# Performance work log

Measured on AMD Instinct MI355X. Metric: run time of the kernel, lower is better.

## Reference

```python
import jax, jax.numpy as jnp
import numpy as np

K = 20
BN_INV = float(1.0 / np.sqrt(1.0 + 1e-5))  # BatchNorm eval with running_mean=0, running_var=1


def _leaky(h):
    return jnp.where(h >= 0, h, 0.2 * h)


def _knn_idx(x, k):
    # x: [B, C, N]; pairwise_distance = -(||xi||^2 + ||xj||^2 - 2 xi.xj); topk = nearest
    inner = jnp.einsum('bcn,bcm->bnm', x, x)
    xx = jnp.sum(x * x, axis=1)  # [B, N]
    pd = 2.0 * inner - xx[:, :, None] - xx[:, None, :]
    return jax.lax.top_k(pd, k)[1]  # [B, N, k]


def _edge_conv(x, w, g, b, k):
    # x: [B, C, N]; w: [Cout, 2C]
    idx = _knn_idx(x, k)
    xt = jnp.transpose(x, (0, 2, 1))  # [B, N, C]
    nb = jax.vmap(lambda f, i: f[i])(xt, idx)  # [B, N, k, C] gathered neighbors
    ctr = xt[:, :, None, :]
    feat = jnp.concatenate([nb - ctr, jnp.broadcast_to(ctr, nb.shape)], axis=-1)  # [B,N,k,2C]
    h = jnp.einsum('bnkc,oc->bnko', feat, w)
    h = _leaky(g * h * BN_INV + b)
    h = jnp.max(h, axis=2)  # max over k neighbors -> [B, N, Cout]
    return jnp.transpose(h, (0, 2, 1))  # [B, Cout, N]


def setup_inputs() -> dict:
    key = jax.random.key(0)
    ks = jax.random.split(key, 32)
    s = 0.05

    def w(i, shape):
        return jax.random.normal(ks[i], shape, dtype=jnp.float32) * s

    def gb(i, c):
        return (1.0 + 0.1 * jax.random.normal(ks[i], (c,), dtype=jnp.float32),
                0.1 * jax.random.normal(jax.random.fold_in(ks[i], 1), (c,), dtype=jnp.float32))

    g1, b1 = gb(1, 64); g2, b2 = gb(2, 64); g3, b3 = gb(3, 128); g4, b4 = gb(4, 256)
    gc, bc = gb(5, 1024); gf1, bf1 = gb(6, 512); gf2, bf2 = gb(7, 256)
    return {
        'x': jax.random.normal(ks[0], (8, 3, 2048), dtype=jnp.float32),
        'w1': w(8, (64, 6)),   'g1': g1, 'b1': b1,
        'w2': w(9, (64, 128)), 'g2': g2, 'b2': b2,
        'w3': w(10, (128, 128)), 'g3': g3, 'b3': b3,
        'w4': w(11, (256, 256)), 'g4': g4, 'b4': b4,
        'wc': w(12, (1024, 512)), 'gc': gc, 'bc': bc,
        'wf1': w(13, (512, 2048)), 'gf1': gf1, 'bf1': bf1,
        'wf2': w(14, (256, 512)), 'bwf2': w(15, (256,)), 'gf2': gf2, 'bf2': bf2,
        'wf3': w(16, (40, 256)), 'bwf3': w(17, (40,)),
    }


def reference(x, w1, g1, b1, w2, g2, b2, w3, g3, b3, w4, g4, b4,
              wc, gc, bc, wf1, gf1, bf1, wf2, bwf2, gf2, bf2, wf3, bwf3):
    x1 = _edge_conv(x, w1, g1, b1, K)   # [B, 64, N]
    x2 = _edge_conv(x1, w2, g2, b2, K)  # [B, 64, N]
    x3 = _edge_conv(x2, w3, g3, b3, K)  # [B, 128, N]
    x4 = _edge_conv(x3, w4, g4, b4, K)  # [B, 256, N]
    h = jnp.concatenate([x1, x2, x3, x4], axis=1)  # [B, 512, N]
    h = jnp.einsum('bcn,oc->bon', h, wc)
    h = _leaky(gc[:, None] * h * BN_INV + bc[:, None])  # [B, 1024, N]
    x5 = jnp.max(h, axis=2)
    x6 = jnp.mean(h, axis=2)
    h = jnp.concatenate([x5, x6], axis=1)  # [B, 2048]
    h = _leaky(gf1 * (h @ wf1.T) * BN_INV + bf1)   # fc1 (no bias) + BN + LeakyReLU
    h = _leaky(gf2 * (h @ wf2.T + bwf2) * BN_INV + bf2)  # fc2 + BN + LeakyReLU (dropout=eval identity)
    return h @ wf3.T + bwf3  # [B, numClass]
```

## Files before the change

kernel.cpp:

```cpp
#include <hip/hip_runtime.h>
#include <hip/hip_bf16.h>
#include <float.h>

#define BB 8
#define NN 2048
#define KK 20

static constexpr float BN_INV_F = 0.9999950000374997f;

typedef __attribute__((ext_vector_type(4))) float f32x4;
typedef __attribute__((ext_vector_type(8))) short s16x8;

__device__ __forceinline__ unsigned short f2bf(float f) {
    __hip_bfloat16 h = __float2bfloat16(f);
    return __builtin_bit_cast(unsigned short, h);
}
__device__ __forceinline__ float bf2f(unsigned short u) {
    unsigned int v = ((unsigned int)u) << 16;
    return __builtin_bit_cast(float, v);
}
__device__ __forceinline__ unsigned mono(float f) {
    unsigned b = __builtin_bit_cast(unsigned, f);
    return b ^ (unsigned)(((int)b >> 31) | 0x80000000);
}

__global__ void split_kernel(const float* __restrict__ w, unsigned short* __restrict__ hi,
                             unsigned short* __restrict__ lo, int n) {
    int t = blockIdx.x * blockDim.x + threadIdx.x;
    if (t >= n) return;
    float v = w[t];
    unsigned short h = f2bf(v);
    hi[t] = h;
    lo[t] = f2bf(v - bf2f(h));
}

__global__ void sqnorm_kernel(const float* __restrict__ x, float* __restrict__ xx, int C) {
    int t = blockIdx.x * blockDim.x + threadIdx.x;
    if (t >= BB * NN) return;
    int b = t / NN, n = t % NN;
    const float* xb = x + (size_t)b * C * NN + n;
    float s = 0.f;
    for (int c = 0; c < C; ++c) {
        float v = xb[(size_t)c * NN];
        s += v * v;
    }
    xx[t] = s;
}

__global__ __launch_bounds__(256, 4) void pd_kernel(const float* __restrict__ x,
                                                    const float* __restrict__ xx,
                                                    float* __restrict__ pd,
                                                    int C, int baseB) {
    __shared__ float ctrT[128][8];
    __shared__ float xns[8];

    int blk = blockIdx.x;
    int chalf = blk & 1;
    int rt = (blk >> 1) & 255;
    int b2 = blk >> 9;
    int b = baseB + b2;
    int rbase = rt * 8;
    int tid = threadIdx.x;
    const float* xb = x + (size_t)b * C * NN;

    for (int i = tid; i < C * 8; i += 256) {
        int c = i >> 3, r = i & 7;
        ctrT[c][r] = xb[(size_t)c * NN + rbase + r];
    }
    if (tid < 8) xns[tid] = xx[b * NN + rbase + tid];
    __syncthreads();

    int m0 = chalf * 1024 + tid * 4;
    float acc[8][4];
    #pragma unroll
    for (int r = 0; r < 8; ++r)
        #pragma unroll
        for (int j = 0; j < 4; ++j) acc[r][j] = 0.f;

    f32x4 xv = *(const f32x4*)(xb + m0);
    for (int c = 0; c + 1 < C; ++c) {
        f32x4 nxt = *(const f32x4*)(xb + (size_t)(c + 1) * NN + m0);
        f32x4 c0 = *(const f32x4*)&ctrT[c][0];
        f32x4 c1 = *(const f32x4*)&ctrT[c][4];
        #pragma unroll
        for (int j = 0; j < 4; ++j) {
            acc[0][j] += c0.x * xv[j]; acc[1][j] += c0.y * xv[j];
            acc[2][j] += c0.z * xv[j]; acc[3][j] += c0.w * xv[j];
            acc[4][j] += c1.x * xv[j]; acc[5][j] += c1.y * xv[j];
            acc[6][j] += c1.z * xv[j]; acc[7][j] += c1.w * xv[j];
        }
        xv = nxt;
    }
    {
        f32x4 c0 = *(const f32x4*)&ctrT[C - 1][0];
        f32x4 c1 = *(const f32x4*)&ctrT[C - 1][4];
        #pragma unroll
        for (int j = 0; j < 4; ++j) {
            acc[0][j] += c0.x * xv[j]; acc[1][j] += c0.y * xv[j];
            acc[2][j] += c0.z * xv[j]; acc[3][j] += c0.w * xv[j];
            acc[4][j] += c1.x * xv[j]; acc[5][j] += c1.y * xv[j];
            acc[6][j] += c1.z * xv[j]; acc[7][j] += c1.w * xv[j];
        }
    }
    f32x4 xm = *(const f32x4*)(xx + (size_t)b * NN + m0);
    #pragma unroll
    for (int r = 0; r < 8; ++r) {
        f32x4 out;
        #pragma unroll
        for (int j = 0; j < 4; ++j)
            out[j] = 2.f * acc[r][j] - xns[r] - xm[j];
        *(f32x4*)&pd[((size_t)(b2 * NN + rbase + r)) * NN + m0] = out;
    }
}

__global__ __launch_bounds__(256, 4) void topk_kernel(const float* __restrict__ pd,
                                                      int* __restrict__ idxout, int baseB) {
    __shared__ unsigned long long cand[4][128];
    int w = threadIdx.x >> 6, lane = threadIdx.x & 63;
    int rowc = blockIdx.x * 4 + w;
    const float* prow = pd + (size_t)rowc * NN;

    float fv[32];
    #pragma unroll
    for (int j4 = 0; j4 < 8; ++j4) {
        f32x4 v = *(const f32x4*)(prow + j4 * 256 + lane * 4);
        #pragma unroll
        for (int e = 0; e < 4; ++e) fv[j4 * 4 + e] = v[e];
    }

    float lm = fv[0];
    #pragma unroll
    for (int i = 1; i < 32; ++i) lm = fmaxf(lm, fv[i]);

    float v = lm;
    #pragma unroll
    for (int k = 2; k <= 64; k <<= 1)
        #pragma unroll
        for (int j = k >> 1; j > 0; j >>= 1) {
            float o = __shfl_xor(v, j, 64);
            bool up = ((lane & k) == 0);
            bool keepMax = up ? ((lane & j) == 0) : ((lane & j) != 0);
            float mx = fmaxf(v, o), mn = fminf(v, o);
            v = keepMax ? mx : mn;
        }
    float Tf = __shfl(v, KK - 1, 64);

    cand[w][lane] = 0ull;
    cand[w][64 + lane] = 0ull;
    __builtin_amdgcn_wave_barrier();
    int base = 0;
    #pragma unroll
    for (int i = 0; i < 32; ++i) {
        int col = (i >> 2) * 256 + lane * 4 + (i & 3);
        bool c = fv[i] >= Tf;
        unsigned long long mask = __ballot(c);
        if (c) {
            int pos = base + (int)__popcll(mask & ((1ull << lane) - 1ull));
            if (pos < 128)
                cand[w][pos] = ((unsigned long long)mono(fv[i]) << 32) | (unsigned)~col;
        }
        base += (int)__popcll(mask);
    }
    __builtin_amdgcn_wave_barrier();

    unsigned long long ka = cand[w][lane];
    auto cmpx = [&](unsigned long long& key, int j, bool up) {
        unsigned long long o = __shfl_xor(key, j, 64);
        bool keepMax = up ? ((lane & j) == 0) : ((lane & j) != 0);
        bool gt = key > o;
        unsigned long long mx = gt ? key : o, mn = gt ? o : key;
        key = keepMax ? mx : mn;
    };
    if (base <= 64) {
        #pragma unroll
        for (int k = 2; k <= 64; k <<= 1)
            #pragma unroll
            for (int j = k >> 1; j > 0; j >>= 1)
                cmpx(ka, j, (lane & k) == 0);
    } else {
        unsigned long long kb = cand[w][64 + lane];
        #pragma unroll
        for (int k = 2; k <= 128; k <<= 1) {
            #pragma unroll
            for (int j = k >> 1; j > 0; j >>= 1) {
                if (j == 64) {
                    unsigned long long mx = ka > kb ? ka : kb;
                    unsigned long long mn = ka > kb ? kb : ka;
                    ka = mx; kb = mn;
                } else {
                    bool upA, upB;
                    if (k == 128)     { upA = true; upB = true; }
                    else if (k == 64) { upA = true; upB = false; }
                    else              { upA = ((lane & k) == 0); upB = upA; }
                    cmpx(ka, j, upA);
                    cmpx(kb, j, upB);
                }
            }
        }
    }

    if (lane < KK) {
        int col = (int)~(unsigned)(ka & 0xFFFFFFFFull);
        int b = baseB + (rowc >> 11);
        int n = rowc & 2047;
        idxout[((size_t)(b * NN + n)) * KK + lane] = col;
    }
}

__global__ __launch_bounds__(256) void pq_gemm_kernel(const float* __restrict__ x,
                                                      const float* __restrict__ w,
                                                      float* __restrict__ Pt, float* __restrict__ Qt,
                                                      int C, int Cout) {
    __shared__ float wPT[128][8];
    __shared__ float wQT[128][8];
    int blk = blockIdx.x;
    int pass = blk & 1;
    int rest = blk >> 1;
    int nog = Cout >> 3;
    int b = rest / nog;
    int obase = (rest % nog) * 8;
    int tid = threadIdx.x;
    const float* xb = x + (size_t)b * C * NN;

    for (int i = tid; i < C * 8; i += 256) {
        int c = i >> 3, r = i & 7;
        wPT[c][r] = w[(size_t)(obase + r) * 2 * C + c];
        wQT[c][r] = w[(size_t)(obase + r) * 2 * C + C + c];
    }
    __syncthreads();

    int m0 = pass * 1024 + tid * 4;
    float aP[8][4], aQ[8][4];
    #pragma unroll
    for (int r = 0; r < 8; ++r)
        #pragma unroll
        for (int j = 0; j < 4; ++j) { aP[r][j] = 0.f; aQ[r][j] = 0.f; }

    for (int c = 0; c < C; ++c) {
        f32x4 xv = *(const f32x4*)(xb + (size_t)c * NN + m0);
        f32x4 p0 = *(const f32x4*)&wPT[c][0];
        f32x4 p1 = *(const f32x4*)&wPT[c][4];
        f32x4 q0 = *(const f32x4*)&wQT[c][0];
        f32x4 q1 = *(const f32x4*)&wQT[c][4];
        #pragma unroll
        for (int j = 0; j < 4; ++j) {
            aP[0][j] += p0.x * xv[j]; aP[1][j] += p0.y * xv[j];
            aP[2][j] += p0.z * xv[j]; aP[3][j] += p0.w * xv[j];
            aP[4][j] += p1.x * xv[j]; aP[5][j] += p1.y * xv[j];
            aP[6][j] += p1.z * xv[j]; aP[7][j] += p1.w * xv[j];
            aQ[0][j] += q0.x * xv[j]; aQ[1][j] += q0.y * xv[j];
            aQ[2][j] += q0.z * xv[j]; aQ[3][j] += q0.w * xv[j];
            aQ[4][j] += q1.x * xv[j]; aQ[5][j] += q1.y * xv[j];
            aQ[6][j] += q1.z * xv[j]; aQ[7][j] += q1.w * xv[j];
        }
    }
    #pragma unroll
    for (int j = 0; j < 4; ++j) {
        size_t base = ((size_t)b * NN + m0 + j) * Cout + obase;
        f32x4 vP0, vP1, vQ0, vQ1;
        #pragma unroll
        for (int r = 0; r < 4; ++r) { vP0[r] = aP[r][j]; vP1[r] = aP[r + 4][j];
                                      vQ0[r] = aQ[r][j]; vQ1[r] = aQ[r + 4][j]; }
        *(f32x4*)&Pt[base] = vP0; *(f32x4*)&Pt[base + 4] = vP1;
        *(f32x4*)&Qt[base] = vQ0; *(f32x4*)&Qt[base + 4] = vQ1;
    }
}

__global__ __launch_bounds__(256) void edge_max_kernel(const float* __restrict__ Pt,
                                                       const float* __restrict__ Qt,
                                                       const int* __restrict__ idx,
                                                       const float* __restrict__ g,
                                                       const float* __restrict__ bt,
                                                       float* __restrict__ xf32,
                                                       unsigned short* __restrict__ Fhi,
                                                       unsigned short* __restrict__ Flo,
                                                       int coff, int Cout) {
    __shared__ int lidx[16][KK];
    int lanesPerN = Cout >> 2;
    int npw = 64 / lanesPerN;
    int nPerBlock = 4 * npw;

    int blk = blockIdx.x;
    int b = blk / (NN / nPerBlock);
    int nbase = (blk % (NN / nPerBlock)) * nPerBlock;
    int tid = threadIdx.x, wid = tid >> 6, lane = tid & 63;

    for (int i = tid; i < nPerBlock * KK; i += 256) {
        int ln = i / KK, k = i % KK;
        lidx[ln][k] = idx[((size_t)(b * NN + nbase + ln)) * KK + k];
    }
    __syncthreads();

    int nsub = lane / lanesPerN;
    int ol = (lane & (lanesPerN - 1)) * 4;
    int nrow = wid * npw + nsub;
    int n = nbase + nrow;

    const float* Pb = Pt + (size_t)b * NN * Cout;
    size_t rowbase = (size_t)n * Cout + ol;
    f32x4 Pn = *(const f32x4*)&Pb[rowbase];
    f32x4 Qn = *(const f32x4*)(Qt + (size_t)b * NN * Cout + rowbase);
    f32x4 off4 = Qn - Pn;
    f32x4 sc4 = *(const f32x4*)&g[ol];
    f32x4 bs4 = *(const f32x4*)&bt[ol];
    #pragma unroll
    for (int e = 0; e < 4; ++e) sc4[e] *= BN_INV_F;

    f32x4 mx4 = { -FLT_MAX, -FLT_MAX, -FLT_MAX, -FLT_MAX };
    #pragma unroll 4
    for (int k = 0; k < KK; ++k) {
        int m = lidx[nrow][k];
        f32x4 pv = *(const f32x4*)&Pb[(size_t)m * Cout + ol];
        #pragma unroll
        for (int e = 0; e < 4; ++e) {
            float y = sc4[e] * (pv[e] + off4[e]) + bs4[e];
            y = (y >= 0.f) ? y : 0.2f * y;
            mx4[e] = fmaxf(mx4[e], y);
        }
    }

    if (xf32) {
        #pragma unroll
        for (int e = 0; e < 4; ++e)
            xf32[((size_t)b * Cout + ol + e) * NN + n] = mx4[e];
    }
    size_t fb = ((size_t)b * NN + n) * 512 + coff + ol;
    ushort4 h4, l4;
    #pragma unroll
    for (int e = 0; e < 4; ++e) {
        unsigned short h = f2bf(mx4[e]);
        ((unsigned short*)&h4)[e] = h;
        ((unsigned short*)&l4)[e] = f2bf(mx4[e] - bf2f(h));
    }
    *(ushort4*)&Fhi[fb] = h4;
    *(ushort4*)&Flo[fb] = l4;
}

__global__ __launch_bounds__(256) void conv_mfma_kernel(const unsigned short* __restrict__ Whi,
                                                        const unsigned short* __restrict__ Wlo,
                                                        const unsigned short* __restrict__ Fhi,
                                                        const unsigned short* __restrict__ Flo,
                                                        const float* __restrict__ gc,
                                                        const float* __restrict__ bc,
                                                        float* __restrict__ pmax,
                                                        float* __restrict__ psum) {
    __shared__ unsigned short As[128 * 64] __attribute__((aligned(16)));
    __shared__ unsigned short Bs[128 * 64] __attribute__((aligned(16)));

    int blk0 = blockIdx.x;
    int blk = (blk0 & 7) * 128 + (blk0 >> 3);

    int nt = blk & 15, ot = (blk >> 4) & 7, b = blk >> 7;
    int obase = ot * 128, nbase = nt * 128;
    int tid = threadIdx.x, lane = tid & 63, wid = tid >> 6;
    int wo = wid >> 1, wn = wid & 1;

    f32x4 acc[4][4];
    #pragma unroll
    for (int m = 0; m < 4; ++m)
        #pragma unroll
        for (int q = 0; q < 4; ++q) acc[m][q] = (f32x4){0.f, 0.f, 0.f, 0.f};

    int srow = tid >> 1, sb = (tid & 1) * 4;

    for (int kt = 0; kt < 24; ++kt) {
        int seg = kt >> 3;
        int kc = (kt & 7) * 64;
        const unsigned short* Asrc = ((seg == 2) ? Wlo : Whi) + (size_t)obase * 512 + kc;
        const unsigned short* Bsrc = ((seg == 1) ? Flo : Fhi) + ((size_t)b * NN + nbase) * 512 + kc;
        __syncthreads();
        #pragma unroll
        for (int s = 0; s < 4; ++s) {
            int slot = sb + s;
            uint4 av = *(const uint4*)(Asrc + (size_t)srow * 512 + slot * 8);
            *(uint4*)(As + srow * 64 + ((slot ^ (srow & 7)) * 8)) = av;
            uint4 bv = *(const uint4*)(Bsrc + (size_t)srow * 512 + slot * 8);
            *(uint4*)(Bs + srow * 64 + ((slot ^ (srow & 7)) * 8)) = bv;
        }
        __syncthreads();
        #pragma unroll
        for (int ks = 0; ks < 2; ++ks) {
            s16x8 af[4], bf[4];
            #pragma unroll
            for (int m = 0; m < 4; ++m) {
                int r = wo * 64 + m * 16 + (lane & 15);
                int slot = (ks * 4 + (lane >> 4)) ^ (r & 7);
                af[m] = *(const s16x8*)(As + r * 64 + slot * 8);
                int r2 = wn * 64 + m * 16 + (lane & 15);
                int slot2 = (ks * 4 + (lane >> 4)) ^ (r2 & 7);
                bf[m] = *(const s16x8*)(Bs + r2 * 64 + slot2 * 8);
            }
            #pragma unroll
            for (int m = 0; m < 4; ++m)
                #pragma unroll
                for (int q = 0; q < 4; ++q)
                    acc[m][q] = __builtin_amdgcn_mfma_f32_16x16x32_bf16(af[m], bf[q], acc[m][q], 0, 0, 0);
        }
    }

    __syncthreads();
    float* redm = (float*)As;
    float* reds = redm + 256;
    #pragma unroll
    for (int m = 0; m < 4; ++m) {
        #pragma unroll
        for (int rg = 0; rg < 4; ++rg) {
            int olocal = wo * 64 + m * 16 + (lane >> 4) * 4 + rg;
            int o = obase + olocal;
            float scv = gc[o] * BN_INV_F, bsv = bc[o];
            float mx = -FLT_MAX, sm = 0.f;
            #pragma unroll
            for (int q = 0; q < 4; ++q) {
                float y = scv * acc[m][q][rg] + bsv;
                y = (y >= 0.f) ? y : 0.2f * y;
                mx = fmaxf(mx, y);
                sm += y;
            }
            #pragma unroll
            for (int d = 1; d < 16; d <<= 1) {
                mx = fmaxf(mx, __shfl_xor(mx, d, 64));
                sm += __shfl_xor(sm, d, 64);
            }
            if ((lane & 15) == 0) {
                redm[wn * 128 + olocal] = mx;
                reds[wn * 128 + olocal] = sm;
            }
        }
    }
    __syncthreads();
    if (tid < 128) {
        float mx = fmaxf(redm[tid], redm[128 + tid]);
        float sm = reds[tid] + reds[128 + tid];
        size_t base = ((size_t)b * 1024 + obase + tid) * 16 + nt;
        pmax[base] = mx;
        psum[base] = sm;
    }
}

__global__ void pool_reduce_kernel(const float* __restrict__ pmax, const float* __restrict__ psum,
                                   float* __restrict__ x56) {
    int t = blockIdx.x * blockDim.x + threadIdx.x;
    if (t >= BB * 1024) return;
    int b = t >> 10, o = t & 1023;
    float mx = -FLT_MAX, sm = 0.f;
    for (int ch = 0; ch < 16; ++ch) {
        mx = fmaxf(mx, pmax[(size_t)t * 16 + ch]);
        sm += psum[(size_t)t * 16 + ch];
    }
    x56[(size_t)b * 2048 + o] = mx;
    x56[(size_t)b * 2048 + 1024 + o] = sm * (1.0f / 2048.0f);
}

__global__ void fc_kernel(const float* __restrict__ in, const float* __restrict__ w,
                          const float* __restrict__ bw, const float* __restrict__ g,
                          const float* __restrict__ bt, float* __restrict__ out,
                          int Cin, int Cout, int mode) {
    int gt = blockIdx.x * blockDim.x + threadIdx.x;
    int wid = gt >> 6;
    int lane = threadIdx.x & 63;
    if (wid >= BB * Cout) return;
    int b = wid / Cout, o = wid % Cout;
    const float* ib = in + (size_t)b * Cin;
    const float* wr = w + (size_t)o * Cin;
    float acc = 0.f;
    for (int c = lane; c < Cin; c += 64) acc += ib[c] * wr[c];
    for (int d = 32; d >= 1; d >>= 1) acc += __shfl_down(acc, d, 64);
    if (lane == 0) {
        float y;
        if (mode == 0)      { y = g[o] * acc * BN_INV_F + bt[o]; y = (y >= 0.f) ? y : 0.2f * y; }
        else if (mode == 1) { float h = acc + bw[o]; y = g[o] * h * BN_INV_F + bt[o]; y = (y >= 0.f) ? y : 0.2f * y; }
        else                { y = acc + bw[o]; }
        out[(size_t)b * Cout + o] = y;
    }
}

extern "C" void kernel_launch(void* const* d_in, const int* in_sizes, int n_in,
                              void* d_out, int out_size, void* d_ws, size_t ws_size,
                              hipStream_t stream) {
    const float* x    = (const float*)d_in[0];
    const float* w1   = (const float*)d_in[1];
    const float* g1   = (const float*)d_in[2];
    const float* b1   = (const float*)d_in[3];
    const float* w2   = (const float*)d_in[4];
    const float* g2   = (const float*)d_in[5];
    const float* b2   = (const float*)d_in[6];
    const float* w3   = (const float*)d_in[7];
    const float* g3   = (const float*)d_in[8];
    const float* b3   = (const float*)d_in[9];
    const float* w4   = (const float*)d_in[10];
    const float* g4   = (const float*)d_in[11];
    const float* b4   = (const float*)d_in[12];
    const float* wc   = (const float*)d_in[13];
    const float* gc   = (const float*)d_in[14];
    const float* bc   = (const float*)d_in[15];
    const float* wf1  = (const float*)d_in[16];
    const float* gf1  = (const float*)d_in[17];
    const float* bf1  = (const float*)d_in[18];
    const float* wf2  = (const float*)d_in[19];
    const float* bwf2 = (const float*)d_in[20];
    const float* gf2  = (const float*)d_in[21];
    const float* bf2  = (const float*)d_in[22];
    const float* wf3  = (const float*)d_in[23];
    const float* bwf3 = (const float*)d_in[24];

    char* ws = (char*)d_ws;
    size_t off = 0;
    auto alloc = [&](size_t nbytes) {
        char* p = ws + off;
        off += (nbytes + 255) & ~(size_t)255;
        return p;
    };
    float* xx   = (float*)alloc((size_t)BB * NN * 4);
    int*   idx  = (int*)  alloc((size_t)BB * NN * KK * 4);
    float* Pt   = (float*)alloc((size_t)BB * NN * 256 * 4);
    float* Qt   = (float*)alloc((size_t)BB * NN * 256 * 4);
    float* x1   = (float*)alloc((size_t)BB * 64 * NN * 4);
    float* x2   = (float*)alloc((size_t)BB * 64 * NN * 4);
    float* x3   = (float*)alloc((size_t)BB * 128 * NN * 4);
    unsigned short* Fhi = (unsigned short*)alloc((size_t)BB * NN * 512 * 2);
    unsigned short* Flo = (unsigned short*)alloc((size_t)BB * NN * 512 * 2);
    unsigned short* Whi = (unsigned short*)alloc((size_t)1024 * 512 * 2);
    unsigned short* Wlo = (unsigned short*)alloc((size_t)1024 * 512 * 2);
    float* pmax = (float*)alloc((size_t)BB * 1024 * 16 * 4);
    float* psum = (float*)alloc((size_t)BB * 1024 * 16 * 4);
    float* x56  = (float*)alloc((size_t)BB * 2048 * 4);
    float* f1   = (float*)alloc((size_t)BB * 512 * 4);
    float* f2   = (float*)alloc((size_t)BB * 256 * 4);

    float* pdbuf = Pt;

    split_kernel<<<(1024 * 512 + 255) / 256, 256, 0, stream>>>(wc, Whi, Wlo, 1024 * 512);

    struct Layer { const float* xin; int C; const float* w; const float* g; const float* bt;
                   float* xout; int Cout; int coff; };
    Layer L[4] = {
        { x,  3,   w1, g1, b1, x1,      64,  0   },
        { x1, 64,  w2, g2, b2, x2,      64,  64  },
        { x2, 64,  w3, g3, b3, x3,      128, 128 },
        { x3, 128, w4, g4, b4, nullptr, 256, 256 },
    };

    for (int l = 0; l < 4; ++l) {
        sqnorm_kernel<<<(BB * NN) / 256, 256, 0, stream>>>(L[l].xin, xx, L[l].C);
        for (int ch = 0; ch < 4; ++ch) {
            pd_kernel<<<1024, 256, 0, stream>>>(L[l].xin, xx, pdbuf, L[l].C, ch * 2);
            topk_kernel<<<1024, 256, 0, stream>>>(pdbuf, idx, ch * 2);
        }
        pq_gemm_kernel<<<BB * (L[l].Cout / 8) * 2, 256, 0, stream>>>(L[l].xin, L[l].w, Pt, Qt, L[l].C, L[l].Cout);
        int nPerBlock = 4 * (64 / (L[l].Cout >> 2));
        edge_max_kernel<<<BB * (NN / nPerBlock), 256, 0, stream>>>(Pt, Qt, idx, L[l].g, L[l].bt,
                                                                   L[l].xout, Fhi, Flo, L[l].coff, L[l].Cout);
    }

    conv_mfma_kernel<<<BB * 8 * 16, 256, 0, stream>>>(Whi, Wlo, Fhi, Flo, gc, bc, pmax, psum);
    pool_reduce_kernel<<<(BB * 1024 + 255) / 256, 256, 0, stream>>>(pmax, psum, x56);
    fc_kernel<<<(BB * 512 * 64 + 255) / 256, 256, 0, stream>>>(x56, wf1, nullptr, gf1, bf1, f1, 2048, 512, 0);
    fc_kernel<<<(BB * 256 * 64 + 255) / 256, 256, 0, stream>>>(f1, wf2, bwf2, gf2, bf2, f2, 512, 256, 1);
    fc_kernel<<<(BB * 40 * 64 + 255) / 256, 256, 0, stream>>>(f2, wf3, bwf3, nullptr, nullptr, (float*)d_out, 256, 40, 2);
}
```

Measured before the change: 849.9 us.

## Emit per-segment maxima in pd kernel to prune top-k row scans

The distance kernel now writes the maximum of every 16-column segment of each row to a small side buffer. Top-k reads those 128 segment maxima, bitonic-sorts them to get a threshold from the 20th largest, and loads only the segments whose maximum reaches that threshold. The goal is to avoid reading every full distance row in top-k. In exchange the pd kernel does extra shuffles and stores, and the candidate loads become scattered, divergent and data-dependent.

```diff
diff --git a/kernel.cpp b/kernel.cpp
--- a/kernel.cpp
+++ b/kernel.cpp
@@ -50,6 +50,7 @@
 __global__ __launch_bounds__(256, 4) void pd_kernel(const float* __restrict__ x,
                                                     const float* __restrict__ xx,
                                                     float* __restrict__ pd,
+                                                    float* __restrict__ smax,
                                                     int C, int baseB) {
     __shared__ float ctrT[128][8];
     __shared__ float xns[8];
@@ -110,60 +111,89 @@
         for (int j = 0; j < 4; ++j)
             out[j] = 2.f * acc[r][j] - xns[r] - xm[j];
         *(f32x4*)&pd[((size_t)(b2 * NN + rbase + r)) * NN + m0] = out;
+        float m4 = fmaxf(fmaxf(out[0], out[1]), fmaxf(out[2], out[3]));
+        m4 = fmaxf(m4, __shfl_xor(m4, 1, 64));
+        m4 = fmaxf(m4, __shfl_xor(m4, 2, 64));
+        if ((tid & 3) == 0)
+            smax[((size_t)(b2 * NN + rbase + r)) * 128 + chalf * 64 + (tid >> 2)] = m4;
     }
 }
 
 __global__ __launch_bounds__(256, 4) void topk_kernel(const float* __restrict__ pd,
+                                                      const float* __restrict__ smax,
                                                       int* __restrict__ idxout, int baseB) {
     __shared__ unsigned long long cand[4][128];
     int w = threadIdx.x >> 6, lane = threadIdx.x & 63;
     int rowc = blockIdx.x * 4 + w;
     const float* prow = pd + (size_t)rowc * NN;
-
-    float fv[32];
-    #pragma unroll
-    for (int j4 = 0; j4 < 8; ++j4) {
-        f32x4 v = *(const f32x4*)(prow + j4 * 256 + lane * 4);
-        #pragma unroll
-        for (int e = 0; e < 4; ++e) fv[j4 * 4 + e] = v[e];
-    }
-
-    float lm = fv[0];
-    #pragma unroll
-    for (int i = 1; i < 32; ++i) lm = fmaxf(lm, fv[i]);
-
-    float v = lm;
-    #pragma unroll
-    for (int k = 2; k <= 64; k <<= 1)
+    const float* srow = smax + (size_t)rowc * 128;
+
+    float sa0 = srow[lane];
+    float sb0 = srow[64 + lane];
+
+    float ka = sa0, kb = sb0;
+    #pragma unroll
+    for (int k = 2; k <= 128; k <<= 1) {
         #pragma unroll
         for (int j = k >> 1; j > 0; j >>= 1) {
-            float o = __shfl_xor(v, j, 64);
-            bool up = ((lane & k) == 0);
-            bool keepMax = up ? ((lane & j) == 0) : ((lane & j) != 0);
-            float mx = fmaxf(v, o), mn = fminf(v, o);
-            v = keepMax ? mx : mn;
-        }
-    float Tf = __shfl(v, KK - 1, 64);
+            if (j == 64) {
+                float mx = fmaxf(ka, kb), mn = fminf(ka, kb);
+                ka = mx; kb = mn;
+            } else {
+                bool upA, upB;
+                if (k == 128)     { upA = true;  upB = true;  }
+                else if (k == 64) { upA = true;  upB = false; }
+                else              { upA = ((lane & k) == 0); upB = upA; }
+                {
+                    float o = __shfl_xor(ka, j, 64);
+                    bool keepMax = upA ? ((lane & j) == 0) : ((lane & j) != 0);
+                    ka = keepMax ? fmaxf(ka, o) : fminf(ka, o);
+                }
+                {
+                    float o = __shfl_xor(kb, j, 64);
+                    bool keepMax = upB ? ((lane & j) == 0) : ((lane & j) != 0);
+                    kb = keepMax ? fmaxf(kb, o) : fminf(kb, o);
+                }
+            }
+        }
+    }
+    float Tf = __shfl(ka, KK - 1, 64);
 
     cand[w][lane] = 0ull;
     cand[w][64 + lane] = 0ull;
     __builtin_amdgcn_wave_barrier();
+
     int base = 0;
     #pragma unroll
-    for (int i = 0; i < 32; ++i) {
-        int col = (i >> 2) * 256 + lane * 4 + (i & 3);
-        bool c = fv[i] >= Tf;
-        unsigned long long mask = __ballot(c);
-        if (c) {
-            int pos = base + (int)__popcll(mask & ((1ull << lane) - 1ull));
-            if (pos < 128)
-                cand[w][pos] = ((unsigned long long)mono(fv[i]) << 32) | (unsigned)~col;
-        }
-        base += (int)__popcll(mask);
+    for (int j = 0; j < 2; ++j) {
+        int seg = j * 64 + lane;
+        float sm = j ? sb0 : sa0;
+        bool active = sm >= Tf;
+        f32x4 v0 = { -FLT_MAX, -FLT_MAX, -FLT_MAX, -FLT_MAX };
+        f32x4 v1 = v0, v2 = v0, v3 = v0;
+        if (active) {
+            const float* sp = prow + seg * 16;
+            v0 = *(const f32x4*)(sp);
+            v1 = *(const f32x4*)(sp + 4);
+            v2 = *(const f32x4*)(sp + 8);
+            v3 = *(const f32x4*)(sp + 12);
+        }
+        #pragma unroll
+        for (int e = 0; e < 16; ++e) {
+            float v = (e < 4) ? v0[e] : (e < 8) ? v1[e - 4] : (e < 12) ? v2[e - 8] : v3[e - 12];
+            bool c = active && (v >= Tf);
+            unsigned long long mask = __ballot(c);
+            if (c) {
+                int pos = base + (int)__popcll(mask & ((1ull << lane) - 1ull));
+                if (pos < 128)
+                    cand[w][pos] = ((unsigned long long)mono(v) << 32) | (unsigned)~(seg * 16 + e);
+            }
+            base += (int)__popcll(mask);
+        }
     }
     __builtin_amdgcn_wave_barrier();
 
-    unsigned long long ka = cand[w][lane];
+    unsigned long long qa = cand[w][lane];
     auto cmpx = [&](unsigned long long& key, int j, bool up) {
         unsigned long long o = __shfl_xor(key, j, 64);
         bool keepMax = up ? ((lane & j) == 0) : ((lane & j) != 0);
@@ -176,31 +206,31 @@
         for (int k = 2; k <= 64; k <<= 1)
             #pragma unroll
             for (int j = k >> 1; j > 0; j >>= 1)
-                cmpx(ka, j, (lane & k) == 0);
+                cmpx(qa, j, (lane & k) == 0);
     } else {
-        unsigned long long kb = cand[w][64 + lane];
+        unsigned long long qb = cand[w][64 + lane];
         #pragma unroll
         for (int k = 2; k <= 128; k <<= 1) {
             #pragma unroll
             for (int j = k >> 1; j > 0; j >>= 1) {
                 if (j == 64) {
-                    unsigned long long mx = ka > kb ? ka : kb;
-                    unsigned long long mn = ka > kb ? kb : ka;
-                    ka = mx; kb = mn;
+                    unsigned long long mx = qa > qb ? qa : qb;
+                    unsigned long long mn = qa > qb ? qb : qa;
+                    qa = mx; qb = mn;
                 } else {
                     bool upA, upB;
                     if (k == 128)     { upA = true; upB = true; }
                     else if (k == 64) { upA = true; upB = false; }
                     else              { upA = ((lane & k) == 0); upB = upA; }
-                    cmpx(ka, j, upA);
-                    cmpx(kb, j, upB);
+                    cmpx(qa, j, upA);
+                    cmpx(qb, j, upB);
                 }
             }
         }
     }
 
     if (lane < KK) {
-        int col = (int)~(unsigned)(ka & 0xFFFFFFFFull);
+        int col = (int)~(unsigned)(qa & 0xFFFFFFFFull);
         int b = baseB + (rowc >> 11);
         int n = rowc & 2047;
         idxout[((size_t)(b * NN + n)) * KK + lane] = col;
@@ -514,6 +544,7 @@
     int*   idx  = (int*)  alloc((size_t)BB * NN * KK * 4);
     float* Pt   = (float*)alloc((size_t)BB * NN * 256 * 4);
     float* Qt   = (float*)alloc((size_t)BB * NN * 256 * 4);
+    float* smax = (float*)alloc((size_t)2 * NN * 128 * 4);
     float* x1   = (float*)alloc((size_t)BB * 64 * NN * 4);
     float* x2   = (float*)alloc((size_t)BB * 64 * NN * 4);
     float* x3   = (float*)alloc((size_t)BB * 128 * NN * 4);
@@ -543,8 +574,8 @@
     for (int l = 0; l < 4; ++l) {
         sqnorm_kernel<<<(BB * NN) / 256, 256, 0, stream>>>(L[l].xin, xx, L[l].C);
         for (int ch = 0; ch < 4; ++ch) {
-            pd_kernel<<<1024, 256, 0, stream>>>(L[l].xin, xx, pdbuf, L[l].C, ch * 2);
-            topk_kernel<<<1024, 256, 0, stream>>>(pdbuf, idx, ch * 2);
+            pd_kernel<<<1024, 256, 0, stream>>>(L[l].xin, xx, pdbuf, smax, L[l].C, ch * 2);
+            topk_kernel<<<1024, 256, 0, stream>>>(pdbuf, smax, idx, ch * 2);
         }
         pq_gemm_kernel<<<BB * (L[l].Cout / 8) * 2, 256, 0, stream>>>(L[l].xin, L[l].w, Pt, Qt, L[l].C, L[l].Cout);
         int nPerBlock = 4 * (64 / (L[l].Cout >> 2));
```

New measurement: 816.0 us (median of 2 runs). 4.0% less time.
